# Performance work log

Measured on AMD Instinct MI355X. Metric: run time of the kernel, lower is better.

Reference implementation:

```python
import jax, jax.numpy as jnp
import numpy as np

D = 1e-6
B, N, E, K = 128, 512, 512, 256


def _lower_median_abs(x, axis):
    # torch.median returns the LOWER of the two middle values for even counts
    n = x.shape[axis]
    s = jnp.sort(jnp.abs(x), axis=axis)
    return jnp.take(s, (n - 1) // 2, axis=axis)


def _bounds_from_cauchy(head, errors, k):
    # errors: (B, E, *head.shape[1:]); E divisible by k in this config
    b, e = errors.shape[0], errors.shape[1]
    tail = errors.shape[2:]
    chunks = errors.reshape(b, e // k, k, *tail)
    l1 = _lower_median_abs(chunks, axis=2).sum(axis=1)
    return head - l1, head + l1


def _relaxed_exp(h, errs, noise, lb, ub):
    is_tight = ub == lb
    lam_s = (jnp.exp(ub) - jnp.exp(lb)) / (ub - lb + D)
    lam = jnp.minimum(lam_s, jnp.exp(lb + 1.0 - 0.1))
    ub0 = jnp.where(lam > lam_s, jnp.exp(lb) - lam * lb, jnp.exp(ub) - lam * ub)
    mu = 0.5 * (lam * (1.0 - jnp.log(lam)) + ub0)
    delta = 0.5 * (ub0 - lam * (1.0 - jnp.log(lam)))
    lam = jnp.where(is_tight, 0.0, lam)
    mu = jnp.where(is_tight, jnp.exp(ub), mu)
    delta = jnp.where(is_tight, 0.0, delta)
    new_head = h * lam + mu
    new_errs = jnp.concatenate([errs * lam[:, None], delta[:, None] * noise], axis=1)
    return new_head, new_errs


def _relaxed_log(h, errs, noise, lb, ub):
    is_tight = ub == lb
    lam_s = (jnp.log(ub) - jnp.log(lb + D)) / (ub - lb + D)
    lam = lam_s
    lb0 = jnp.where(lam < lam_s, jnp.log(ub) - ub * lam, jnp.log(lb + D) - lb * lam)
    mu = 0.5 * (-jnp.log(lam) - 1.0 + lb0)
    delta = 0.5 * (-jnp.log(lam) - 1.0 - lb0)
    lam = jnp.where(is_tight, 0.0, lam)
    mu = jnp.where(is_tight, jnp.log(ub), mu)
    delta = jnp.where(is_tight, 0.0, delta)
    new_head = h * lam + mu
    new_errs = jnp.concatenate([errs * lam[:, None], delta[:, None] * noise], axis=1)
    return new_head, new_errs


def setup_inputs() -> dict:
    key = jax.random.key(0)
    k1, k2, k3, k4 = jax.random.split(key, 4)
    curr_head = jax.random.normal(k1, (B, N), dtype=jnp.float32)
    # small error magnitudes keep exp/log relaxation bounds valid (lb of log stage > 0)
    curr_errors = 1e-3 * jax.random.normal(k2, (B * E, N), dtype=jnp.float32)
    cauchy_exp = jax.random.cauchy(k3, (B, K, N), dtype=jnp.float32)
    cauchy_log = jax.random.cauchy(k4, (B, K), dtype=jnp.float32)
    return {"curr_head": curr_head, "curr_errors": curr_errors,
            "cauchy_exp": cauchy_exp, "cauchy_log": cauchy_log, "k": K}


def reference(curr_head, curr_errors, cauchy_exp, cauchy_log, k):
    b, n = curr_head.shape
    max_head = jax.lax.stop_gradient(jnp.max(curr_head, axis=1, keepdims=True))  # (B,1)
    temp_head = curr_head - max_head                         # (B,N)
    errs = curr_errors.reshape(b, -1, n)                     # (B,E,N)
    lb, ub = _bounds_from_cauchy(temp_head, errs, k)
    exp_head, exp_errs = _relaxed_exp(temp_head, errs, cauchy_exp, lb, ub)  # (B,N),(B,E+K,N)
    exp_head = exp_head.sum(axis=1)                          # (B,)
    exp_errs = exp_errs.sum(axis=2)                          # (B,E+K)
    lb2, ub2 = _bounds_from_cauchy(exp_head, exp_errs, k)
    ls_head, ls_errs = _relaxed_log(exp_head, exp_errs, cauchy_log, lb2, ub2)  # (B,),(B,E+2K)
    ls_head = ls_head + max_head[:, 0]
    return ls_head, ls_errs.reshape(-1)
```

## Files before the change

kernel.cpp:

```cpp
#include <hip/hip_runtime.h>
#include <cstdint>
#include <cstddef>

#define BB 128
#define NN 512
#define EE 512
#define KK 256
#define STR 17

__device__ __forceinline__ float wave_reduce_max(float v) {
#pragma unroll
  for (int off = 32; off >= 1; off >>= 1) v = fmaxf(v, __shfl_xor(v, off, 64));
  return v;
}
__device__ __forceinline__ float wave_reduce_sum(float v) {
#pragma unroll
  for (int off = 32; off >= 1; off >>= 1) v += __shfl_xor(v, off, 64);
  return v;
}

__device__ __forceinline__ float wave_median256(float a0, float a1, float a2, float a3) {
  float m = fmaxf(fmaxf(a0, a1), fmaxf(a2, a3));
  m = wave_reduce_max(m);
  float hi = __uint_as_float(__float_as_uint(m) + 1u);
  float lo = 0.f;
  float pivot = hi;
  bool found = false;
  for (int it = 0; it < 40; ++it) {
    pivot = 0.5f * (lo + hi);
    int cnt = __popcll(__ballot(a0 < pivot)) + __popcll(__ballot(a1 < pivot)) +
              __popcll(__ballot(a2 < pivot)) + __popcll(__ballot(a3 < pivot));
    if (cnt == 128) { found = true; break; }
    if (cnt < 128) lo = pivot; else hi = pivot;
  }
  float p = found ? pivot : hi;
  float s0 = (a0 < p) ? a0 : 0.f;
  float s1 = (a1 < p) ? a1 : 0.f;
  float s2 = (a2 < p) ? a2 : 0.f;
  float s3 = (a3 < p) ? a3 : 0.f;
  return wave_reduce_max(fmaxf(fmaxf(s0, s1), fmaxf(s2, s3)));
}

__global__ __launch_bounds__(256, 4) void kfused(
    const float* __restrict__ head, const float* __restrict__ errs,
    float* __restrict__ ws_delta, float* __restrict__ ws_htpart,
    float* __restrict__ ws_epart) {
  __shared__ float tile[512 * STR];
  __shared__ float medbuf[32];
  __shared__ float lambuf[16];
  __shared__ float redm[4];
  const int blk = blockIdx.x;
  const int b = blk >> 5, g = blk & 31;
  const int n0 = g * 16;
  const int tid = threadIdx.x, wave = tid >> 6, lane = tid & 63;

  float m = fmaxf(head[(size_t)b * NN + tid], head[(size_t)b * NN + 256 + tid]);
  m = wave_reduce_max(m);
  if (lane == 0) redm[wave] = m;

  const int tr = tid >> 2, tc = (tid & 3) * 4;
  const float* src = errs + (size_t)b * EE * NN + n0 + tc;
#pragma unroll
  for (int i = 0; i < 8; ++i) {
    int row = i * 64 + tr;
    float4 v = *(const float4*)(src + (size_t)row * NN);
    float* dst = &tile[row * STR + tc];
    dst[0] = v.x; dst[1] = v.y; dst[2] = v.z; dst[3] = v.w;
  }
  __syncthreads();
  float hmax = fmaxf(fmaxf(redm[0], redm[1]), fmaxf(redm[2], redm[3]));

#pragma unroll 1
  for (int jj = 0; jj < 8; ++jj) {
    int p = wave * 8 + jj;
    int col = p & 15;
    int rb = (p >> 4) * 256;
    float a0 = fabsf(tile[(rb + lane) * STR + col]);
    float a1 = fabsf(tile[(rb + lane + 64) * STR + col]);
    float a2 = fabsf(tile[(rb + lane + 128) * STR + col]);
    float a3 = fabsf(tile[(rb + lane + 192) * STR + col]);
    float med = wave_median256(a0, a1, a2, a3);
    if (lane == 0) medbuf[p] = med;
  }
  __syncthreads();

  float htp = 0.f;
  if (tid < 16) {
    int n = n0 + tid;
    float l1 = medbuf[tid] + medbuf[16 + tid];
    float th = head[(size_t)b * NN + n] - hmax;
    float lb = th - l1, ub = th + l1;
    float lam, mu, delta;
    if (ub == lb) {
      lam = 0.f; mu = expf(ub); delta = 0.f;
    } else {
      float elb = expf(lb), eub = expf(ub);
      float lam_s = (eub - elb) / (ub - lb + 1e-6f);
      lam = fminf(lam_s, expf(lb + 0.9f));
      float ub0 = (lam > lam_s) ? (elb - lam * lb) : (eub - lam * ub);
      float t = lam * (1.f - logf(lam));
      mu = 0.5f * (t + ub0);
      delta = 0.5f * (ub0 - t);
    }
    lambuf[tid] = lam;
    ws_delta[(size_t)b * NN + n] = delta;
    htp = th * lam + mu;
  }
  if (wave == 0) {
    float s = wave_reduce_sum(htp);
    if (lane == 0) ws_htpart[b * 32 + g] = s;
  }
  __syncthreads();

  float s0 = 0.f, s1 = 0.f;
#pragma unroll
  for (int j = 0; j < 16; ++j) {
    float w = lambuf[j];
    s0 = fmaf(tile[tid * STR + j], w, s0);
    s1 = fmaf(tile[(tid + 256) * STR + j], w, s1);
  }
  float* op = ws_epart + ((size_t)(b * 32 + g)) * 512;
  op[tid] = s0;
  op[tid + 256] = s1;
}

__global__ __launch_bounds__(256) void kcexp(
    const float* __restrict__ cexp, const float* __restrict__ ws_delta,
    float* __restrict__ ws_ee2) {
  const int blk = blockIdx.x;
  const int b = blk >> 2, part = blk & 3;
  const int wave = threadIdx.x >> 6, lane = threadIdx.x & 63;
  const float* wsrc = ws_delta + (size_t)b * NN;
  float4 wa = *(const float4*)(wsrc + 4 * lane);
  float4 wb = *(const float4*)(wsrc + 256 + 4 * lane);
  const int r0 = part * 64 + wave * 16;
  const float* base = cexp + (size_t)b * KK * NN;
  float* out = ws_ee2 + (size_t)b * KK;
#pragma unroll 1
  for (int i = 0; i < 16; ++i) {
    int r = r0 + i;
    const float* rp = base + (size_t)r * NN;
    float4 x = *(const float4*)(rp + 4 * lane);
    float4 y = *(const float4*)(rp + 256 + 4 * lane);
    float s = x.x * wa.x + x.y * wa.y + x.z * wa.z + x.w * wa.w +
              y.x * wb.x + y.y * wb.y + y.z * wb.z + y.w * wb.w;
    s = wave_reduce_sum(s);
    if (lane == 0) out[r] = s;
  }
}

__global__ __launch_bounds__(256) void kstage3(
    const float* __restrict__ head, const float* __restrict__ clog,
    const float* __restrict__ ws_htpart, const float* __restrict__ ws_epart,
    const float* __restrict__ ws_ee2, float* __restrict__ out) {
  __shared__ float eb[768];
  __shared__ float redm[4];
  __shared__ float meds[3];
  __shared__ float sc[2];
  __shared__ float ehsh;
  const int b = blockIdx.x;
  const int tid = threadIdx.x, wave = tid >> 6, lane = tid & 63;

  float m = fmaxf(head[(size_t)b * NN + tid], head[(size_t)b * NN + 256 + tid]);
  m = wave_reduce_max(m);
  if (lane == 0) redm[wave] = m;

  float acc0 = 0.f, acc1 = 0.f;
  const float* pp = ws_epart + (size_t)b * 32 * 512;
#pragma unroll
  for (int g = 0; g < 32; ++g) {
    acc0 += pp[g * 512 + tid];
    acc1 += pp[g * 512 + 256 + tid];
  }
  eb[tid] = acc0;
  eb[tid + 256] = acc1;
  eb[512 + tid >= 768 ? 0 : 512 + tid] = ws_ee2[(size_t)b * KK + tid];
  __syncthreads();

  if (wave < 3) {
    const float* p = eb + wave * 256;
    float a0 = fabsf(p[lane]), a1 = fabsf(p[lane + 64]);
    float a2 = fabsf(p[lane + 128]), a3 = fabsf(p[lane + 192]);
    float med = wave_median256(a0, a1, a2, a3);
    if (lane == 0) meds[wave] = med;
  } else {
    float v = (lane < 32) ? ws_htpart[b * 32 + lane] : 0.f;
    v = wave_reduce_sum(v);
    if (lane == 0) ehsh = v;
  }
  __syncthreads();

  if (tid == 0) {
    float hmax = fmaxf(fmaxf(redm[0], redm[1]), fmaxf(redm[2], redm[3]));
    float eh = ehsh;
    float l1 = meds[0] + meds[1] + meds[2];
    float lb = eh - l1, ub = eh + l1;
    float lam, mu, delta;
    if (ub == lb) {
      lam = 0.f; mu = logf(ub); delta = 0.f;
    } else {
      float llb = logf(lb + 1e-6f);
      float lam_s = (logf(ub) - llb) / (ub - lb + 1e-6f);
      lam = lam_s;
      float lb0 = llb - lb * lam;
      float t = -logf(lam) - 1.f;
      mu = 0.5f * (t + lb0);
      delta = 0.5f * (t - lb0);
    }
    sc[0] = lam; sc[1] = delta;
    out[b] = eh * lam + mu + hmax;
  }
  __syncthreads();
  float lam = sc[0], delta = sc[1];
  float* ob = out + BB + (size_t)b * 1024;
  ob[tid] = eb[tid] * lam;
  ob[tid + 256] = eb[tid + 256] * lam;
  ob[tid + 512] = eb[tid + 512] * lam;
  ob[tid + 768] = delta * clog[(size_t)b * KK + tid];
}

extern "C" void kernel_launch(void* const* d_in, const int* in_sizes, int n_in,
                              void* d_out, int out_size, void* d_ws, size_t ws_size,
                              hipStream_t stream) {
  const float* head = (const float*)d_in[0];
  const float* errs = (const float*)d_in[1];
  const float* cexp = (const float*)d_in[2];
  const float* clog = (const float*)d_in[3];
  float* out = (float*)d_out;

  float* ws = (float*)d_ws;
  float* ws_delta = ws;
  float* ws_htpart = ws_delta + BB * NN;
  float* ws_ee2 = ws_htpart + BB * 32;
  float* ws_epart = ws_ee2 + BB * KK;

  hipLaunchKernelGGL(kfused, dim3(BB * 32), dim3(256), 0, stream,
                     head, errs, ws_delta, ws_htpart, ws_epart);
  hipLaunchKernelGGL(kcexp, dim3(BB * 4), dim3(256), 0, stream,
                     cexp, ws_delta, ws_ee2);
  hipLaunchKernelGGL(kstage3, dim3(BB), dim3(256), 0, stream,
                     head, clog, ws_htpart, ws_epart, ws_ee2, out);
}
```

Measured before the change: 274.8 us.

## Replace bisection median with mean-seeded interpolation search using DPP reductions

The lower-median selection over 256 values per wave now seeds its pivot from the wave mean, then uses secant-style interpolation on counts before falling back to bisection, instead of plain bisection from the maximum. It also accepts a count of 127 by taking the minimum of the values at or above the pivot. The goal is to cut the number of ballot/popcount iterations in the median loops that dominate the fused kernel. Reductions switch from shfl_xor to DPP row operations plus readlane, which lowers per-reduction latency. The pivot heuristic is tuned to the input distribution and adds more branching per iteration.

New measurement: 270.4 us. About the same (-1.6%).

```diff
diff --git a/kernel.cpp b/kernel.cpp
--- a/kernel.cpp
+++ b/kernel.cpp
@@ -19,26 +19,66 @@
   return v;
 }
 
-__device__ __forceinline__ float wave_median256(float a0, float a1, float a2, float a3) {
-  float m = fmaxf(fmaxf(a0, a1), fmaxf(a2, a3));
-  m = wave_reduce_max(m);
-  float hi = __uint_as_float(__float_as_uint(m) + 1u);
-  float lo = 0.f;
-  float pivot = hi;
-  bool found = false;
-  for (int it = 0; it < 40; ++it) {
-    pivot = 0.5f * (lo + hi);
-    int cnt = __popcll(__ballot(a0 < pivot)) + __popcll(__ballot(a1 < pivot)) +
-              __popcll(__ballot(a2 < pivot)) + __popcll(__ballot(a3 < pivot));
-    if (cnt == 128) { found = true; break; }
-    if (cnt < 128) lo = pivot; else hi = pivot;
-  }
-  float p = found ? pivot : hi;
-  float s0 = (a0 < p) ? a0 : 0.f;
-  float s1 = (a1 < p) ? a1 : 0.f;
-  float s2 = (a2 < p) ? a2 : 0.f;
-  float s3 = (a3 < p) ? a3 : 0.f;
-  return wave_reduce_max(fmaxf(fmaxf(s0, s1), fmaxf(s2, s3)));
+template <int CTRL>
+__device__ __forceinline__ float dppz(float x) {
+  return __int_as_float(__builtin_amdgcn_update_dpp(0, __float_as_int(x), CTRL, 0xf, 0xf, false));
+}
+template <int CTRL>
+__device__ __forceinline__ float dppi(float x) {
+  return __int_as_float(__builtin_amdgcn_update_dpp(__float_as_int(x), __float_as_int(x), CTRL, 0xf, 0xf, false));
+}
+__device__ __forceinline__ float wave_sum64(float x) {
+  x += dppz<0x111>(x); x += dppz<0x112>(x); x += dppz<0x114>(x); x += dppz<0x118>(x);
+  x += dppz<0x142>(x); x += dppz<0x143>(x);
+  return __int_as_float(__builtin_amdgcn_readlane(__float_as_int(x), 63));
+}
+__device__ __forceinline__ float wave_max64nn(float x) {
+  x = fmaxf(x, dppz<0x111>(x)); x = fmaxf(x, dppz<0x112>(x));
+  x = fmaxf(x, dppz<0x114>(x)); x = fmaxf(x, dppz<0x118>(x));
+  x = fmaxf(x, dppz<0x142>(x)); x = fmaxf(x, dppz<0x143>(x));
+  return __int_as_float(__builtin_amdgcn_readlane(__float_as_int(x), 63));
+}
+__device__ __forceinline__ float wave_min64(float x) {
+  x = fminf(x, dppi<0x111>(x)); x = fminf(x, dppi<0x112>(x));
+  x = fminf(x, dppi<0x114>(x)); x = fminf(x, dppi<0x118>(x));
+  x = fminf(x, dppi<0x142>(x)); x = fminf(x, dppi<0x143>(x));
+  return __int_as_float(__builtin_amdgcn_readlane(__float_as_int(x), 63));
+}
+
+__device__ __forceinline__ float wave_median256_fast(float a0, float a1, float a2, float a3) {
+  float S = wave_sum64((a0 + a1) + (a2 + a3));
+  float mean = S * 0.00390625f;
+  float lo = 0.f, hi = S * 1.0000002f + 1e-37f;
+  int c_lo = 0, c_hi = 256;
+  float piv = 0.845f * mean;
+  float ans = 0.f;
+  bool have = false;
+#pragma unroll 1
+  for (int it = 0; it < 34; ++it) {
+    if (!(piv > lo && piv < hi)) piv = 0.5f * (lo + hi);
+    int cnt = __popcll(__ballot(a0 < piv)) + __popcll(__ballot(a1 < piv)) +
+              __popcll(__ballot(a2 < piv)) + __popcll(__ballot(a3 < piv));
+    if (cnt == 128) {
+      float m = fmaxf(fmaxf(a0 < piv ? a0 : 0.f, a1 < piv ? a1 : 0.f),
+                      fmaxf(a2 < piv ? a2 : 0.f, a3 < piv ? a3 : 0.f));
+      ans = wave_max64nn(m); have = true; break;
+    }
+    if (cnt == 127) {
+      float m = fminf(fminf(a0 >= piv ? a0 : 3.4e38f, a1 >= piv ? a1 : 3.4e38f),
+                      fminf(a2 >= piv ? a2 : 3.4e38f, a3 >= piv ? a3 : 3.4e38f));
+      ans = wave_min64(m); have = true; break;
+    }
+    if (cnt < 127) { lo = piv; c_lo = cnt; } else { hi = piv; c_hi = cnt; }
+    if (it == 0) piv = piv + (127.5f - (float)cnt) * mean * 0.0077f;
+    else piv = lo + (hi - lo) * ((127.5f - (float)c_lo) / (float)(c_hi - c_lo));
+    if (it >= 10) piv = 0.5f * (lo + hi);
+  }
+  if (!have) {
+    float m = fmaxf(fmaxf(a0 < hi ? a0 : 0.f, a1 < hi ? a1 : 0.f),
+                    fmaxf(a2 < hi ? a2 : 0.f, a3 < hi ? a3 : 0.f));
+    ans = wave_max64nn(m);
+  }
+  return ans;
 }
 
 __global__ __launch_bounds__(256, 4) void kfused(
@@ -71,15 +111,15 @@
   float hmax = fmaxf(fmaxf(redm[0], redm[1]), fmaxf(redm[2], redm[3]));
 
 #pragma unroll 1
-  for (int jj = 0; jj < 8; ++jj) {
-    int p = wave * 8 + jj;
+  for (int j = 0; j < 8; ++j) {
+    int p = wave * 8 + j;
     int col = p & 15;
     int rb = (p >> 4) * 256;
     float a0 = fabsf(tile[(rb + lane) * STR + col]);
     float a1 = fabsf(tile[(rb + lane + 64) * STR + col]);
     float a2 = fabsf(tile[(rb + lane + 128) * STR + col]);
     float a3 = fabsf(tile[(rb + lane + 192) * STR + col]);
-    float med = wave_median256(a0, a1, a2, a3);
+    float med = wave_median256_fast(a0, a1, a2, a3);
     if (lane == 0) medbuf[p] = med;
   }
   __syncthreads();
@@ -174,14 +214,14 @@
   }
   eb[tid] = acc0;
   eb[tid + 256] = acc1;
-  eb[512 + tid >= 768 ? 0 : 512 + tid] = ws_ee2[(size_t)b * KK + tid];
+  eb[tid + 512] = ws_ee2[(size_t)b * KK + tid];
   __syncthreads();
 
   if (wave < 3) {
     const float* p = eb + wave * 256;
     float a0 = fabsf(p[lane]), a1 = fabsf(p[lane + 64]);
     float a2 = fabsf(p[lane + 128]), a3 = fabsf(p[lane + 192]);
-    float med = wave_median256(a0, a1, a2, a3);
+    float med = wave_median256_fast(a0, a1, a2, a3);
     if (lane == 0) meds[wave] = med;
   } else {
     float v = (lane < 32) ? ws_htpart[b * 32 + lane] : 0.f;
```
